# Kernel optimization log

Hardware: AMD Instinct MI355X
Metric: run time of the kernel (lower is better)

The kernel has to match this reference:

```python
import jax, jax.numpy as jnp
import numpy as np
from jax import lax

STRIDE = 2  # down_sample_stride
MATMUL_NORM = True


def maxpool2d_5d(x, s):
    # x: [B, T, C, H, W]; kernel=s, stride=s, padding=(s-1)//2 == 0 for s=2
    return lax.reduce_window(
        x, -jnp.inf, lax.max,
        window_dimensions=(1, 1, 1, s, s),
        window_strides=(1, 1, 1, s, s),
        padding='VALID')


def setup_inputs() -> dict:
    key = jax.random.key(0)
    k1, k2, k3, k4 = jax.random.split(key, 4)
    B, T, Ck, Cv, H, W = 2, 4, 64, 256, 64, 64
    return {
        'memory_keys': jax.random.normal(k1, (B, T, Ck, H, W), jnp.float32),
        'memory_values': jax.random.normal(k2, (B, T, Cv, H, W), jnp.float32),
        'query_key': jax.random.normal(k3, (B, Ck, H, W), jnp.float32),
        'query_value': jax.random.normal(k4, (B, Cv, H, W), jnp.float32),
    }


def reference(memory_keys, memory_values, query_key, query_value):
    B, T, Ck, oH, oW = memory_keys.shape
    Cv = memory_values.shape[2]
    # down-sample memory bank (max pool, stride 2, no padding)
    mk = maxpool2d_5d(memory_keys, STRIDE)   # [B,T,Ck,h,w]
    mv = maxpool2d_5d(memory_values, STRIDE) # [B,T,Cv,h,w]
    h, w = mk.shape[-2], mk.shape[-1]
    M = T * h * w
    N = oH * oH  # code uses ori_height*ori_height (square assumed)
    # permute(0,2,1,3,4).view(B,Ck,M).permute(0,2,1) -> [B, M, Ck]
    mk = mk.transpose(0, 2, 1, 3, 4).reshape(B, Ck, M).transpose(0, 2, 1)
    qk = query_key.reshape(B, Ck, N)
    attn = jnp.einsum('bmc,bcn->bmn', mk, qk)  # [B, M, N]
    if MATMUL_NORM:
        attn = attn * (Ck ** -0.5)
    attn = jax.nn.softmax(attn, axis=1)  # softmax over memory positions
    mv = mv.transpose(0, 2, 1, 3, 4).reshape(B, Cv, M)
    memory = jnp.einsum('bcm,bmn->bcn', mv, attn).reshape(B, Cv, oH, oW)
    return jnp.concatenate([query_value, memory], axis=1)  # [B, 2*Cv, H, W]
```

## Files before the change

kernel.cpp:

```cpp
#include <hip/hip_runtime.h>
#include <hip/hip_bf16.h>

typedef unsigned short u16;
typedef unsigned int   u32;
typedef __attribute__((ext_vector_type(8))) short  bf16x8;
typedef __attribute__((ext_vector_type(4))) float  floatx4;

#define NB 2
#define NT 4
#define CK 64
#define CV 256
#define HH 64
#define WW 64
#define MM 4096
#define NN 4096
#define SCALE 0.125f
#define SHIFT 4.0f
#define OUT_B 2097152
#define MSPLIT 2
#define MHALF 2048
#define ITERS 16

__device__ __forceinline__ u16 f2b(float f) {
    __hip_bfloat16 h = __float2bfloat16(f);
    union { __hip_bfloat16 h; u16 u; } v; v.h = h; return v.u;
}


#define KTOT (NB*MM*CK)
__global__ void pool_kv(const float* __restrict__ mk, const float* __restrict__ mv,
                        u16* __restrict__ pk, u16* __restrict__ vt) {
    int e = blockIdx.x * 256 + threadIdx.x;
    if (e < KTOT) {
        int m = e & 4095; int c = (e >> 12) & 63; int b = e >> 18;
        int ww = m & 31, hh = (m >> 5) & 31, t = m >> 10;
        const float* s = mk + ((size_t)(((b*NT + t)*CK + c)*HH + 2*hh))*WW + 2*ww;
        pk[((size_t)b*MM + m)*CK + c] =
            f2b(fmaxf(fmaxf(s[0], s[1]), fmaxf(s[WW], s[WW+1])));
    } else {
        int e2 = e - KTOT;
        int m = e2 & 4095; int c = (e2 >> 12) & 255; int b = e2 >> 20;
        int ww = m & 31, hh = (m >> 5) & 31, t = m >> 10;
        const float* s = mv + ((size_t)(((b*NT + t)*CV + c)*HH + 2*hh))*WW + 2*ww;
        vt[((size_t)b*CV + c)*MM + m] =
            f2b(fmaxf(fmaxf(s[0], s[1]), fmaxf(s[WW], s[WW+1])));
    }
}

__launch_bounds__(512)
__global__ void attn_mfma(const u16* __restrict__ pk, const u16* __restrict__ vt,
                          const float* __restrict__ qk,
                          float* __restrict__ part, float* __restrict__ sums) {
    const int ntile = blockIdx.x, b = blockIdx.y, ms = blockIdx.z;
    const int tid = threadIdx.x, w = tid >> 6, l = tid & 63;
    const int lrow = l & 15, quad = l >> 4;
    const int n0 = ntile * 64;
    const int m0 = ms * MHALF;

    __shared__ u16  P[64 * 128];
    __shared__ float sums_s[8][64];

    bf16x8 qf[2][4];
    const float* qb = qk + (size_t)b * CK * NN;
    #pragma unroll
    for (int cc = 0; cc < 2; ++cc)
        #pragma unroll
        for (int t = 0; t < 4; ++t) {
            int n = n0 + t*16 + lrow;
            #pragma unroll
            for (int i = 0; i < 8; ++i) {
                int c = cc*32 + quad*8 + i;
                qf[cc][t][i] = (short)f2b(qb[(size_t)c*NN + n]);
            }
        }

    const u16* pkb = pk + (size_t)b * MM * CK;
    const u16* vtb = vt + (size_t)b * CV * MM;

    floatx4 oacc[2][4];
    #pragma unroll
    for (int j = 0; j < 2; ++j)
        #pragma unroll
        for (int t = 0; t < 4; ++t)
            oacc[j][t] = (floatx4){0.f, 0.f, 0.f, 0.f};
    float sacc[4] = {0.f, 0.f, 0.f, 0.f};

    const int sw = lrow << 1;

    for (int it = 0; it < ITERS; ++it) {
        const int mbase = m0 + it * 128;

        const u16* kp = pkb + (size_t)(mbase + w*16 + lrow)*CK + quad*8;
        bf16x8 kf0 = *(const bf16x8*)(kp);
        bf16x8 kf1 = *(const bf16x8*)(kp + 32);

        bf16x8 vf[4][2];
        #pragma unroll
        for (int j = 0; j < 2; ++j) {
            const u16* vp = vtb + (size_t)(w*32 + j*16 + lrow)*MM + mbase + quad*8;
            vf[0][j] = *(const bf16x8*)(vp);
            vf[1][j] = *(const bf16x8*)(vp + 32);
            vf[2][j] = *(const bf16x8*)(vp + 64);
            vf[3][j] = *(const bf16x8*)(vp + 96);
        }

        #pragma unroll
        for (int t = 0; t < 4; ++t) {
            floatx4 s = __builtin_amdgcn_mfma_f32_16x16x32_bf16(
                            kf0, qf[0][t], (floatx4){0.f,0.f,0.f,0.f}, 0, 0, 0);
            s = __builtin_amdgcn_mfma_f32_16x16x32_bf16(kf1, qf[1][t], s, 0, 0, 0);
            float p0 = __expf(s[0]*SCALE - SHIFT);
            float p1 = __expf(s[1]*SCALE - SHIFT);
            float p2 = __expf(s[2]*SCALE - SHIFT);
            float p3 = __expf(s[3]*SCALE - SHIFT);
            sacc[t] += (p0 + p1) + (p2 + p3);
            u32 d0 = (u32)f2b(p0) | ((u32)f2b(p1) << 16);
            u32 d1 = (u32)f2b(p2) | ((u32)f2b(p3) << 16);
            int n_l = t*16 + lrow;
            int cb  = (w << 2) + quad;
            *(uint2*)&P[n_l*128 + ((cb ^ sw) << 2)] = make_uint2(d0, d1);
        }
        __syncthreads();

        #pragma unroll
        for (int cc = 0; cc < 4; ++cc) {
            bf16x8 pf[4];
            #pragma unroll
            for (int t = 0; t < 4; ++t) {
                int n_l = t*16 + lrow;
                int cb  = (cc << 3) + (quad << 1);
                pf[t] = *(const bf16x8*)&P[n_l*128 + ((cb ^ sw) << 2)];
            }
            #pragma unroll
            for (int j = 0; j < 2; ++j)
                #pragma unroll
                for (int t = 0; t < 4; ++t)
                    oacc[j][t] = __builtin_amdgcn_mfma_f32_16x16x32_bf16(
                                     vf[cc][j], pf[t], oacc[j][t], 0, 0, 0);
        }
        __syncthreads();
    }

    #pragma unroll
    for (int t = 0; t < 4; ++t) {
        float v = sacc[t];
        v += __shfl_xor(v, 16, 64);
        v += __shfl_xor(v, 32, 64);
        if (l < 16) sums_s[w][t*16 + l] = v;
    }
    __syncthreads();

    float* pb = part + ((size_t)((ms*NB + b)*64 + ntile)) * (256*64);
    #pragma unroll
    for (int j = 0; j < 2; ++j)
        #pragma unroll
        for (int t = 0; t < 4; ++t)
            #pragma unroll
            for (int r = 0; r < 4; ++r) {
                int c = w*32 + j*16 + quad*4 + r;
                int n = t*16 + lrow;
                pb[c*64 + n] = oacc[j][t][r];
            }
    if (tid < 64) {
        float sv = 0.f;
        #pragma unroll
        for (int ww2 = 0; ww2 < 8; ++ww2) sv += sums_s[ww2][tid];
        sums[((size_t)((ms*NB + b)*64 + ntile))*64 + tid] = sv;
    }
}

__global__ void epilogue(const float* __restrict__ part, const float* __restrict__ sums,
                         const float4* __restrict__ qv, float* __restrict__ out) {
    int e = blockIdx.x * 256 + threadIdx.x;
    if (e < 524288) {
        int b = e >> 18; int ru = e & 262143;
        ((float4*)out)[(size_t)b*(OUT_B/4) + ru] = qv[e];
    } else {
        int e4 = e - 524288;
        int nl4   = e4 & 15;
        int ntile = (e4 >> 4) & 63;
        int c     = (e4 >> 10) & 255;
        int b     = e4 >> 18;
        size_t t0 = (size_t)(0*NB + b)*64 + ntile;
        size_t t1 = (size_t)(1*NB + b)*64 + ntile;
        const float4* p4 = (const float4*)part;
        const float4* s4 = (const float4*)sums;
        float4 u0 = p4[t0*4096 + c*16 + nl4];
        float4 u1 = p4[t1*4096 + c*16 + nl4];
        float4 d0 = s4[t0*16 + nl4];
        float4 d1 = s4[t1*16 + nl4];
        float4 r;
        r.x = (u0.x + u1.x) / (d0.x + d1.x);
        r.y = (u0.y + u1.y) / (d0.y + d1.y);
        r.z = (u0.z + u1.z) / (d0.z + d1.z);
        r.w = (u0.w + u1.w) / (d0.w + d1.w);
        ((float4*)out)[(size_t)(b*512 + 256 + c)*1024 + ntile*16 + nl4] = r;
    }
}


__global__ void pool_v_f32(const float* __restrict__ src, float* __restrict__ out) {
    int e = blockIdx.x * 256 + threadIdx.x;
    int c = e & 255;
    int r = e >> 8;
    int ww = r & 31;  int hh = (r >> 5) & 31;
    int t  = (r >> 10) & 3;  int b = r >> 12;
    int m  = r & (MM - 1);
    const float* s = src + ((size_t)(((b*NT + t)*CV + c)*HH + 2*hh))*WW + 2*ww;
    out[(size_t)b*OUT_B + (size_t)m*CV + c] = fmaxf(fmaxf(s[0], s[1]), fmaxf(s[WW], s[WW+1]));
}

__global__ void pool_k_f32(const float* __restrict__ src, float* __restrict__ dst) {
    int e = blockIdx.x * 256 + threadIdx.x;
    int c = e & 63;
    int r = e >> 6;
    int ww = r & 31;  int hh = (r >> 5) & 31;
    int t  = (r >> 10) & 3;  int b = r >> 12;
    const float* s = src + ((size_t)(((b*NT + t)*CK + c)*HH + 2*hh))*WW + 2*ww;
    dst[e] = fmaxf(fmaxf(s[0], s[1]), fmaxf(s[WW], s[WW+1]));
}

__global__ void copy_qv_f32(const float4* __restrict__ src, float4* __restrict__ dst) {
    int u = blockIdx.x * 256 + threadIdx.x;
    int b  = u >> 18;
    int ru = u & 262143;
    dst[(size_t)b * (OUT_B/4) + ru] = src[u];
}

template<bool STAGED_K>
__launch_bounds__(256)
__global__ void attn_old(const float* __restrict__ pk,
                         const float* __restrict__ mk,
                         const float* __restrict__ qk,
                         float* __restrict__ out) {
    __shared__ __align__(16) float q_lds[CK][4];
    __shared__ __align__(16) float sarr[4][MM];
    __shared__ float inv_l[4];

    const int tid = threadIdx.x;
    const int blk = blockIdx.x;
    const int b   = blk >> 10;
    const int n0  = (blk & 1023) << 2;

    {
        int c = tid >> 2, qi = tid & 3;
        q_lds[c][qi] = qk[((size_t)(b*CK + c))*NN + n0 + qi];
    }
    __syncthreads();

    #pragma unroll
    for (int i = 0; i < 16; ++i) {
        int m = tid + (i << 8);
        float a0 = 0.f, a1 = 0.f, a2 = 0.f, a3 = 0.f;
        if (STAGED_K) {
            const float4* k4 = reinterpret_cast<const float4*>(pk + ((size_t)b*MM + m)*CK);
            #pragma unroll
            for (int cc = 0; cc < 16; ++cc) {
                float4 kv = k4[cc];
                int c = cc*4;
                float4 q0 = *reinterpret_cast<const float4*>(&q_lds[c][0]);
                float4 q1 = *reinterpret_cast<const float4*>(&q_lds[c+1][0]);
                float4 q2 = *reinterpret_cast<const float4*>(&q_lds[c+2][0]);
                float4 q3 = *reinterpret_cast<const float4*>(&q_lds[c+3][0]);
                a0 += kv.x*q0.x + kv.y*q1.x + kv.z*q2.x + kv.w*q3.x;
                a1 += kv.x*q0.y + kv.y*q1.y + kv.z*q2.y + kv.w*q3.y;
                a2 += kv.x*q0.z + kv.y*q1.z + kv.z*q2.z + kv.w*q3.z;
                a3 += kv.x*q0.w + kv.y*q1.w + kv.z*q2.w + kv.w*q3.w;
            }
        } else {
            int ww = m & 31, hh = (m >> 5) & 31, t = m >> 10;
            const float* base = mk + ((size_t)((b*NT + t)*CK)*HH + 2*hh)*WW + 2*ww;
            for (int c = 0; c < CK; ++c) {
                const float* s = base + (size_t)c*HH*WW;
                float kv = fmaxf(fmaxf(s[0], s[1]), fmaxf(s[WW], s[WW+1]));
                float4 q = *reinterpret_cast<const float4*>(&q_lds[c][0]);
                a0 += kv*q.x; a1 += kv*q.y; a2 += kv*q.z; a3 += kv*q.w;
            }
        }
        sarr[0][m] = a0*SCALE;
        sarr[1][m] = a1*SCALE;
        sarr[2][m] = a2*SCALE;
        sarr[3][m] = a3*SCALE;
    }
    __syncthreads();

    const int wave = tid >> 6, lane = tid & 63;
    float mx = -3.0e38f;
    for (int m = lane; m < MM; m += 64) mx = fmaxf(mx, sarr[wave][m]);
    #pragma unroll
    for (int off = 32; off > 0; off >>= 1) mx = fmaxf(mx, __shfl_xor(mx, off, 64));
    float ls = 0.f;
    for (int m = lane; m < MM; m += 64) {
        float p = __expf(sarr[wave][m] - mx);
        sarr[wave][m] = p;
        ls += p;
    }
    #pragma unroll
    for (int off = 32; off > 0; off >>= 1) ls += __shfl_xor(ls, off, 64);
    if (lane == 0) inv_l[wave] = 1.0f / ls;
    __syncthreads();

    const int c4 = lane;
    const float4* vb = reinterpret_cast<const float4*>(out + (size_t)b*OUT_B) + c4;
    const float* prow = sarr[wave];
    float a0 = 0.f, a1 = 0.f, a2 = 0.f, a3 = 0.f;
    for (int m = 0; m < MM; m += 4) {
        float4 p4 = *reinterpret_cast<const float4*>(prow + m);
        const float4* vp = vb + (size_t)m*(CV/4);
        float4 v0 = vp[0], v1 = vp[CV/4], v2 = vp[CV/2], v3 = vp[3*(CV/4)];
        a0 += p4.x*v0.x + p4.y*v1.x + p4.z*v2.x + p4.w*v3.x;
        a1 += p4.x*v0.y + p4.y*v1.y + p4.z*v2.y + p4.w*v3.y;
        a2 += p4.x*v0.z + p4.y*v1.z + p4.z*v2.z + p4.w*v3.z;
        a3 += p4.x*v0.w + p4.y*v1.w + p4.z*v2.w + p4.w*v3.w;
    }

    float inv = inv_l[wave];
    int n = n0 + wave;
    size_t ob = ((size_t)(b*512 + 256 + c4*4))*NN + n;
    out[ob]        = a0*inv;
    out[ob + NN]   = a1*inv;
    out[ob + 2*NN] = a2*inv;
    out[ob + 3*NN] = a3*inv;
}


extern "C" void kernel_launch(void* const* d_in, const int* in_sizes, int n_in,
                              void* d_out, int out_size, void* d_ws, size_t ws_size,
                              hipStream_t stream) {
    const float* mk = (const float*)d_in[0];
    const float* mv = (const float*)d_in[1];
    const float* qk = (const float*)d_in[2];
    const float* qv = (const float*)d_in[3];
    float* out = (float*)d_out;

    u16* pk_bf = (u16*)d_ws;
    u16* vt_bf = pk_bf + (size_t)NB*MM*CK;
    float* part = (float*)(vt_bf + (size_t)NB*CV*MM);
    float* sums = part + 4194304;
    const size_t need = (size_t)NB*MM*CK*2 + (size_t)NB*CV*MM*2
                      + (4194304 + 16384) * sizeof(float);

    if (ws_size >= need) {
        pool_kv<<<(KTOT + NB*MM*CV)/256, 256, 0, stream>>>(mk, mv, pk_bf, vt_bf);
        attn_mfma<<<dim3(64, NB, MSPLIT), 512, 0, stream>>>(pk_bf, vt_bf, qk, part, sums);
        epilogue<<<(2*524288)/256, 256, 0, stream>>>(part, sums, (const float4*)qv, out);
    } else {
        const size_t pk_bytes = (size_t)NB*MM*CK*sizeof(float);
        const bool staged = (ws_size >= pk_bytes);
        float* pk = (float*)d_ws;
        pool_v_f32<<<(NB*MM*CV)/256, 256, 0, stream>>>(mv, out);
        if (staged) {
            pool_k_f32<<<(NB*MM*CK)/256, 256, 0, stream>>>(mk, pk);
            attn_old<true ><<<NB*(NN/4), 256, 0, stream>>>(pk, mk, qk, out);
        } else {
            attn_old<false><<<NB*(NN/4), 256, 0, stream>>>(pk, mk, qk, out);
        }
        copy_qv_f32<<<((NB*CV*HH*WW)/4)/256, 256, 0, stream>>>((const float4*)qv, (float4*)out);
    }
}
```

Baseline: 148.6 us.

## Fuse pooling prep with qv copy, remove M-split, and pipeline attention loop

The pooling kernel is rewritten with vectorized loads and a channel-blocked K layout, and it now also performs the query_value copy. The attention kernel drops the two-way M split and the partial-sum buffers. It uses 32-wide N tiles over 256 blocks with XCD-aware block mapping, and normalizes and writes the output directly, which removes the separate epilogue kernel and its workspace round trip. The main loop is software-pipelined with double-buffered LDS, prefetching the next K/V fragments and overlapping QK/exp with PV MFMAs. It also uses s_setprio. The cost is a longer serial M loop per block and more register pressure under launch_bounds(512,2).

```diff
diff --git a/kernel.cpp b/kernel.cpp
--- a/kernel.cpp
+++ b/kernel.cpp
@@ -17,185 +17,209 @@
 #define SCALE 0.125f
 #define SHIFT 4.0f
 #define OUT_B 2097152
-#define MSPLIT 2
-#define MHALF 2048
-#define ITERS 16
+#define NW 32
+#define NIT 32
 
 __device__ __forceinline__ u16 f2b(float f) {
     __hip_bfloat16 h = __float2bfloat16(f);
     union { __hip_bfloat16 h; u16 u; } v; v.h = h; return v.u;
 }
 
-
-#define KTOT (NB*MM*CK)
-__global__ void pool_kv(const float* __restrict__ mk, const float* __restrict__ mv,
-                        u16* __restrict__ pk, u16* __restrict__ vt) {
-    int e = blockIdx.x * 256 + threadIdx.x;
-    if (e < KTOT) {
-        int m = e & 4095; int c = (e >> 12) & 63; int b = e >> 18;
-        int ww = m & 31, hh = (m >> 5) & 31, t = m >> 10;
-        const float* s = mk + ((size_t)(((b*NT + t)*CK + c)*HH + 2*hh))*WW + 2*ww;
-        pk[((size_t)b*MM + m)*CK + c] =
-            f2b(fmaxf(fmaxf(s[0], s[1]), fmaxf(s[WW], s[WW+1])));
+#define PRE_K 65536
+#define PRE_V 589824
+#define PRE_T 1114112
+
+__global__ void prep(const float* __restrict__ mk, const float* __restrict__ mv,
+                     const float4* __restrict__ qv,
+                     u16* __restrict__ pk2, u16* __restrict__ vt,
+                     float* __restrict__ out) {
+    int u = blockIdx.x * 256 + threadIdx.x;
+    if (u < PRE_K) {
+        int m = u & 4095, cb8 = (u >> 12) & 7, b = u >> 15;
+        int t = m >> 10, hh = (m >> 5) & 31, ww = m & 31;
+        const float* s0 = mk + ((size_t)((b*NT + t)*CK + cb8*8))*(HH*WW)
+                             + (2*hh)*WW + 2*ww;
+        bf16x8 fr;
+        #pragma unroll
+        for (int i = 0; i < 8; ++i) {
+            const float* s = s0 + (size_t)i*(HH*WW);
+            float2 r0 = *(const float2*)s;
+            float2 r1 = *(const float2*)(s + WW);
+            fr[i] = (short)f2b(fmaxf(fmaxf(r0.x, r0.y), fmaxf(r1.x, r1.y)));
+        }
+        *(bf16x8*)(pk2 + ((size_t)(b*8 + cb8)*MM + m)*8) = fr;
+    } else if (u < PRE_V) {
+        int u2 = u - PRE_K;
+        int m4 = u2 & 1023, c = (u2 >> 10) & 255, b = u2 >> 18;
+        int t = m4 >> 8, hh = (m4 >> 3) & 31, w8 = m4 & 7;
+        const float* s0 = mv + ((size_t)((b*NT + t)*CV + c))*(HH*WW)
+                             + (2*hh)*WW + 8*w8;
+        float4 a0 = *(const float4*)(s0);
+        float4 a1 = *(const float4*)(s0 + 4);
+        float4 b0 = *(const float4*)(s0 + WW);
+        float4 b1 = *(const float4*)(s0 + WW + 4);
+        ushort4 r;
+        r.x = f2b(fmaxf(fmaxf(a0.x, a0.y), fmaxf(b0.x, b0.y)));
+        r.y = f2b(fmaxf(fmaxf(a0.z, a0.w), fmaxf(b0.z, b0.w)));
+        r.z = f2b(fmaxf(fmaxf(a1.x, a1.y), fmaxf(b1.x, b1.y)));
+        r.w = f2b(fmaxf(fmaxf(a1.z, a1.w), fmaxf(b1.z, b1.w)));
+        *(ushort4*)(vt + ((size_t)(b*CV + c)*MM) + m4*4) = r;
     } else {
-        int e2 = e - KTOT;
-        int m = e2 & 4095; int c = (e2 >> 12) & 255; int b = e2 >> 20;
-        int ww = m & 31, hh = (m >> 5) & 31, t = m >> 10;
-        const float* s = mv + ((size_t)(((b*NT + t)*CV + c)*HH + 2*hh))*WW + 2*ww;
-        vt[((size_t)b*CV + c)*MM + m] =
-            f2b(fmaxf(fmaxf(s[0], s[1]), fmaxf(s[WW], s[WW+1])));
-    }
-}
-
-__launch_bounds__(512)
-__global__ void attn_mfma(const u16* __restrict__ pk, const u16* __restrict__ vt,
-                          const float* __restrict__ qk,
-                          float* __restrict__ part, float* __restrict__ sums) {
-    const int ntile = blockIdx.x, b = blockIdx.y, ms = blockIdx.z;
+        int u3 = u - PRE_V;
+        int b = u3 >> 18, ru = u3 & 262143;
+        ((float4*)out)[(size_t)b*(OUT_B/4) + ru] = qv[u3];
+    }
+}
+
+__device__ __forceinline__ void qk_phase(bf16x8 k0, bf16x8 k1,
+        const bf16x8 (&qf)[2][2], float (&sacc)[2],
+        u16* __restrict__ Pd, int lrow, int cbw, int sw)
+{
+    #pragma unroll
+    for (int t = 0; t < 2; ++t) {
+        floatx4 s = __builtin_amdgcn_mfma_f32_16x16x32_bf16(
+                        k0, qf[0][t], (floatx4){0.f,0.f,0.f,0.f}, 0, 0, 0);
+        s = __builtin_amdgcn_mfma_f32_16x16x32_bf16(k1, qf[1][t], s, 0, 0, 0);
+        float p0 = __expf(s[0]*SCALE - SHIFT);
+        float p1 = __expf(s[1]*SCALE - SHIFT);
+        float p2 = __expf(s[2]*SCALE - SHIFT);
+        float p3 = __expf(s[3]*SCALE - SHIFT);
+        sacc[t] += (p0 + p1) + (p2 + p3);
+        u32 d0 = (u32)f2b(p0) | ((u32)f2b(p1) << 16);
+        u32 d1 = (u32)f2b(p2) | ((u32)f2b(p3) << 16);
+        *(uint2*)&Pd[(t*16 + lrow)*128 + ((cbw ^ sw) << 2)] = make_uint2(d0, d1);
+    }
+}
+
+__device__ __forceinline__ void pv_phase(const bf16x8 (&vf)[4][2],
+        floatx4 (&oacc)[2][2], const u16* __restrict__ Ps,
+        int lrow, int quad, int sw)
+{
+    #pragma unroll
+    for (int cc = 0; cc < 4; ++cc) {
+        bf16x8 pf[2];
+        #pragma unroll
+        for (int t = 0; t < 2; ++t) {
+            int cb = (cc << 3) + (quad << 1);
+            pf[t] = *(const bf16x8*)&Ps[(t*16 + lrow)*128 + ((cb ^ sw) << 2)];
+        }
+        __builtin_amdgcn_s_setprio(1);
+        #pragma unroll
+        for (int j = 0; j < 2; ++j)
+            #pragma unroll
+            for (int t = 0; t < 2; ++t)
+                oacc[j][t] = __builtin_amdgcn_mfma_f32_16x16x32_bf16(
+                                 vf[cc][j], pf[t], oacc[j][t], 0, 0, 0);
+        __builtin_amdgcn_s_setprio(0);
+    }
+}
+
+__launch_bounds__(512, 2)
+__global__ void attn_v2(const u16* __restrict__ pk2, const u16* __restrict__ vt,
+                        const float* __restrict__ qk, float* __restrict__ out) {
+    const int bid = blockIdx.x;
+    const int xcd = bid & 7;
+    const int b   = xcd >> 2;
+    const int ntile = ((bid >> 3) << 2) + (xcd & 3);
     const int tid = threadIdx.x, w = tid >> 6, l = tid & 63;
     const int lrow = l & 15, quad = l >> 4;
-    const int n0 = ntile * 64;
-    const int m0 = ms * MHALF;
-
-    __shared__ u16  P[64 * 128];
-    __shared__ float sums_s[8][64];
-
-    bf16x8 qf[2][4];
-    const float* qb = qk + (size_t)b * CK * NN;
+    const int n0 = ntile * NW;
+    const int sw = lrow << 1;
+    const int cbw = (w << 2) + quad;
+
+    __shared__ u16  P[2][NW * 128];
+    __shared__ float sums_s[8][NW];
+
+    bf16x8 qf[2][2];
+    const float* qb = qk + (size_t)b * CK * NN + n0;
     #pragma unroll
     for (int cc = 0; cc < 2; ++cc)
         #pragma unroll
-        for (int t = 0; t < 4; ++t) {
-            int n = n0 + t*16 + lrow;
+        for (int t = 0; t < 2; ++t)
             #pragma unroll
             for (int i = 0; i < 8; ++i) {
                 int c = cc*32 + quad*8 + i;
-                qf[cc][t][i] = (short)f2b(qb[(size_t)c*NN + n]);
+                qf[cc][t][i] = (short)f2b(qb[(size_t)c*NN + t*16 + lrow]);
             }
-        }
-
-    const u16* pkb = pk + (size_t)b * MM * CK;
-    const u16* vtb = vt + (size_t)b * CV * MM;
-
-    floatx4 oacc[2][4];
+
+    const u16* pkb  = pk2 + (size_t)b * (8*MM*8);
+    const u16* vtb  = vt  + (size_t)b * CV * MM;
+    const int  mrw  = w*16 + lrow;
+    const u16* vrow = vtb + (size_t)(w*32 + lrow)*MM + quad*8;
+
+    floatx4 oacc[2][2];
     #pragma unroll
     for (int j = 0; j < 2; ++j)
         #pragma unroll
-        for (int t = 0; t < 4; ++t)
+        for (int t = 0; t < 2; ++t)
             oacc[j][t] = (floatx4){0.f, 0.f, 0.f, 0.f};
-    float sacc[4] = {0.f, 0.f, 0.f, 0.f};
-
-    const int sw = lrow << 1;
-
-    for (int it = 0; it < ITERS; ++it) {
-        const int mbase = m0 + it * 128;
-
-        const u16* kp = pkb + (size_t)(mbase + w*16 + lrow)*CK + quad*8;
-        bf16x8 kf0 = *(const bf16x8*)(kp);
-        bf16x8 kf1 = *(const bf16x8*)(kp + 32);
-
-        bf16x8 vf[4][2];
-        #pragma unroll
-        for (int j = 0; j < 2; ++j) {
-            const u16* vp = vtb + (size_t)(w*32 + j*16 + lrow)*MM + mbase + quad*8;
-            vf[0][j] = *(const bf16x8*)(vp);
-            vf[1][j] = *(const bf16x8*)(vp + 32);
-            vf[2][j] = *(const bf16x8*)(vp + 64);
-            vf[3][j] = *(const bf16x8*)(vp + 96);
-        }
-
-        #pragma unroll
-        for (int t = 0; t < 4; ++t) {
-            floatx4 s = __builtin_amdgcn_mfma_f32_16x16x32_bf16(
-                            kf0, qf[0][t], (floatx4){0.f,0.f,0.f,0.f}, 0, 0, 0);
-            s = __builtin_amdgcn_mfma_f32_16x16x32_bf16(kf1, qf[1][t], s, 0, 0, 0);
-            float p0 = __expf(s[0]*SCALE - SHIFT);
-            float p1 = __expf(s[1]*SCALE - SHIFT);
-            float p2 = __expf(s[2]*SCALE - SHIFT);
-            float p3 = __expf(s[3]*SCALE - SHIFT);
-            sacc[t] += (p0 + p1) + (p2 + p3);
-            u32 d0 = (u32)f2b(p0) | ((u32)f2b(p1) << 16);
-            u32 d1 = (u32)f2b(p2) | ((u32)f2b(p3) << 16);
-            int n_l = t*16 + lrow;
-            int cb  = (w << 2) + quad;
-            *(uint2*)&P[n_l*128 + ((cb ^ sw) << 2)] = make_uint2(d0, d1);
-        }
+    float sacc[2] = {0.f, 0.f};
+
+    bf16x8 vf[4][2];
+    {
+        bf16x8 k0 = *(const bf16x8*)(pkb + ((size_t)quad*MM + mrw)*8);
+        bf16x8 k1 = *(const bf16x8*)(pkb + ((size_t)(quad+4)*MM + mrw)*8);
+        #pragma unroll
+        for (int cc = 0; cc < 4; ++cc)
+            #pragma unroll
+            for (int j = 0; j < 2; ++j)
+                vf[cc][j] = *(const bf16x8*)(vrow + (size_t)j*(16*MM) + cc*32);
+        qk_phase(k0, k1, qf, sacc, P[0], lrow, cbw, sw);
+    }
+
+    #pragma unroll 2
+    for (int it = 0; it < NIT; ++it) {
         __syncthreads();
-
-        #pragma unroll
-        for (int cc = 0; cc < 4; ++cc) {
-            bf16x8 pf[4];
-            #pragma unroll
-            for (int t = 0; t < 4; ++t) {
-                int n_l = t*16 + lrow;
-                int cb  = (cc << 3) + (quad << 1);
-                pf[t] = *(const bf16x8*)&P[n_l*128 + ((cb ^ sw) << 2)];
-            }
-            #pragma unroll
-            for (int j = 0; j < 2; ++j)
+        const bool more = (it + 1 < NIT);
+        bf16x8 k0n, k1n, vfn[4][2];
+        if (more) {
+            const int mb2 = (it + 1) << 7;
+            k0n = *(const bf16x8*)(pkb + ((size_t)quad*MM + mb2 + mrw)*8);
+            k1n = *(const bf16x8*)(pkb + ((size_t)(quad+4)*MM + mb2 + mrw)*8);
+            #pragma unroll
+            for (int cc = 0; cc < 4; ++cc)
                 #pragma unroll
-                for (int t = 0; t < 4; ++t)
-                    oacc[j][t] = __builtin_amdgcn_mfma_f32_16x16x32_bf16(
-                                     vf[cc][j], pf[t], oacc[j][t], 0, 0, 0);
-        }
-        __syncthreads();
-    }
-
-    #pragma unroll
-    for (int t = 0; t < 4; ++t) {
+                for (int j = 0; j < 2; ++j)
+                    vfn[cc][j] = *(const bf16x8*)(vrow + (size_t)j*(16*MM) + mb2 + cc*32);
+        }
+        pv_phase(vf, oacc, P[it & 1], lrow, quad, sw);
+        if (more) {
+            qk_phase(k0n, k1n, qf, sacc, P[(it + 1) & 1], lrow, cbw, sw);
+            #pragma unroll
+            for (int cc = 0; cc < 4; ++cc)
+                #pragma unroll
+                for (int j = 0; j < 2; ++j)
+                    vf[cc][j] = vfn[cc][j];
+        }
+    }
+
+    #pragma unroll
+    for (int t = 0; t < 2; ++t) {
         float v = sacc[t];
         v += __shfl_xor(v, 16, 64);
         v += __shfl_xor(v, 32, 64);
         if (l < 16) sums_s[w][t*16 + l] = v;
     }
     __syncthreads();
-
-    float* pb = part + ((size_t)((ms*NB + b)*64 + ntile)) * (256*64);
+    float inv[2];
+    #pragma unroll
+    for (int t = 0; t < 2; ++t) {
+        float d = 0.f;
+        #pragma unroll
+        for (int w2 = 0; w2 < 8; ++w2) d += sums_s[w2][t*16 + lrow];
+        inv[t] = 1.0f / d;
+    }
+
+    float* ob = out + ((size_t)(b*512 + 256))*NN + n0;
     #pragma unroll
     for (int j = 0; j < 2; ++j)
         #pragma unroll
-        for (int t = 0; t < 4; ++t)
+        for (int t = 0; t < 2; ++t)
             #pragma unroll
             for (int r = 0; r < 4; ++r) {
                 int c = w*32 + j*16 + quad*4 + r;
-                int n = t*16 + lrow;
-                pb[c*64 + n] = oacc[j][t][r];
+                ob[(size_t)c*NN + t*16 + lrow] = oacc[j][t][r] * inv[t];
             }
-    if (tid < 64) {
-        float sv = 0.f;
-        #pragma unroll
-        for (int ww2 = 0; ww2 < 8; ++ww2) sv += sums_s[ww2][tid];
-        sums[((size_t)((ms*NB + b)*64 + ntile))*64 + tid] = sv;
-    }
-}
-
-__global__ void epilogue(const float* __restrict__ part, const float* __restrict__ sums,
-                         const float4* __restrict__ qv, float* __restrict__ out) {
-    int e = blockIdx.x * 256 + threadIdx.x;
-    if (e < 524288) {
-        int b = e >> 18; int ru = e & 262143;
-        ((float4*)out)[(size_t)b*(OUT_B/4) + ru] = qv[e];
-    } else {
-        int e4 = e - 524288;
-        int nl4   = e4 & 15;
-        int ntile = (e4 >> 4) & 63;
-        int c     = (e4 >> 10) & 255;
-        int b     = e4 >> 18;
-        size_t t0 = (size_t)(0*NB + b)*64 + ntile;
-        size_t t1 = (size_t)(1*NB + b)*64 + ntile;
-        const float4* p4 = (const float4*)part;
-        const float4* s4 = (const float4*)sums;
-        float4 u0 = p4[t0*4096 + c*16 + nl4];
-        float4 u1 = p4[t1*4096 + c*16 + nl4];
-        float4 d0 = s4[t0*16 + nl4];
-        float4 d1 = s4[t1*16 + nl4];
-        float4 r;
-        r.x = (u0.x + u1.x) / (d0.x + d1.x);
-        r.y = (u0.y + u1.y) / (d0.y + d1.y);
-        r.z = (u0.z + u1.z) / (d0.z + d1.z);
-        r.w = (u0.w + u1.w) / (d0.w + d1.w);
-        ((float4*)out)[(size_t)(b*512 + 256 + c)*1024 + ntile*16 + nl4] = r;
-    }
 }
 
 
@@ -333,17 +357,13 @@
     const float* qv = (const float*)d_in[3];
     float* out = (float*)d_out;
 
-    u16* pk_bf = (u16*)d_ws;
-    u16* vt_bf = pk_bf + (size_t)NB*MM*CK;
-    float* part = (float*)(vt_bf + (size_t)NB*CV*MM);
-    float* sums = part + 4194304;
-    const size_t need = (size_t)NB*MM*CK*2 + (size_t)NB*CV*MM*2
-                      + (4194304 + 16384) * sizeof(float);
+    u16* pk2 = (u16*)d_ws;
+    u16* vt  = pk2 + (size_t)NB*8*MM*8;
+    const size_t need = ((size_t)NB*8*MM*8 + (size_t)NB*CV*MM) * sizeof(u16);
 
     if (ws_size >= need) {
-        pool_kv<<<(KTOT + NB*MM*CV)/256, 256, 0, stream>>>(mk, mv, pk_bf, vt_bf);
-        attn_mfma<<<dim3(64, NB, MSPLIT), 512, 0, stream>>>(pk_bf, vt_bf, qk, part, sums);
-        epilogue<<<(2*524288)/256, 256, 0, stream>>>(part, sums, (const float4*)qv, out);
+        prep<<<PRE_T/256, 256, 0, stream>>>(mk, mv, (const float4*)qv, pk2, vt, out);
+        attn_v2<<<256, 512, 0, stream>>>(pk2, vt, qk, out);
     } else {
         const size_t pk_bytes = (size_t)NB*MM*CK*sizeof(float);
         const bool staged = (ws_size >= pk_bytes);
```

Result: slower. 161.0 us (+8.3%).
